# Kernel tuning notes

Hardware: AMD Instinct MI355X
Metric: run time of the kernel (lower is better)

## Reference

```python
import jax, jax.numpy as jnp
import numpy as np

EMBED_DIM = 512
POS_DIM = 192
NUM_HEADS = 8
QUERY_HEAD_DIM = 32
POS_HEAD_DIM = 4
SEQ_LEN = 1024
BATCH = 8
IN_PROJ_DIM = (QUERY_HEAD_DIM * 2 + POS_HEAD_DIM) * NUM_HEADS  # 544


def setup_inputs() -> dict:
    key = jax.random.key(0)
    ks = jax.random.split(key, 5)
    x = jax.random.normal(ks[0], (SEQ_LEN, BATCH, EMBED_DIM), dtype=jnp.float32)
    pos_emb = jax.random.normal(ks[1], (1, 2 * SEQ_LEN - 1, POS_DIM), dtype=jnp.float32)
    key_padding_mask = jnp.zeros((BATCH, SEQ_LEN), dtype=bool)
    # ScaledLinear(embed_dim, in_proj_dim) with initial_scale=query_head_dim**-0.25
    in_proj_w = jax.random.normal(ks[2], (IN_PROJ_DIM, EMBED_DIM), dtype=jnp.float32) * (EMBED_DIM ** -0.5) * (QUERY_HEAD_DIM ** -0.25)
    in_proj_b = jax.random.normal(ks[3], (IN_PROJ_DIM,), dtype=jnp.float32) * 0.01
    # ScaledLinear(pos_dim, num_heads*pos_head_dim, bias=False, initial_scale=0.05)
    linear_pos_w = jax.random.normal(ks[4], (NUM_HEADS * POS_HEAD_DIM, POS_DIM), dtype=jnp.float32) * (POS_DIM ** -0.5) * 0.05
    return {"x": x, "pos_emb": pos_emb, "key_padding_mask": key_padding_mask,
            "in_proj_w": in_proj_w, "in_proj_b": in_proj_b, "linear_pos_w": linear_pos_w}


def reference(x, pos_emb, key_padding_mask, in_proj_w, in_proj_b, linear_pos_w):
    S, B, _ = x.shape
    H, QD, PD = NUM_HEADS, QUERY_HEAD_DIM, POS_HEAD_DIM
    proj = jnp.einsum('sbe,oe->sbo', x, in_proj_w) + in_proj_b  # (S,B,544)
    qdim = H * QD
    q = proj[..., :qdim].reshape(S, B, H, QD).transpose(2, 1, 0, 3)          # (H,B,S,QD)
    k = proj[..., qdim:2 * qdim].reshape(S, B, H, QD).transpose(2, 1, 3, 0)  # (H,B,QD,S)
    p = proj[..., 2 * qdim:].reshape(S, B, H, PD).transpose(2, 1, 0, 3)      # (H,B,S,PD)
    attn_scores = jnp.matmul(q, k)  # (H,B,S,S)
    # positional scores
    pe = jnp.einsum('ltd,od->lto', pos_emb, linear_pos_w)                    # (1,2S-1,H*PD)
    pe = pe.reshape(1, 2 * S - 1, H, PD).transpose(2, 0, 3, 1)               # (H,1,PD,2S-1)
    pos_scores = jnp.matmul(p, pe)                                           # (H,B,S,2S-1)
    # rel-shift: out[h,b,i,j] = pos_scores[h,b,i, (S-1) + j - i]
    idx = (S - 1) + jnp.arange(S)[None, :] - jnp.arange(S)[:, None]          # (S,S)
    pos_scores = jnp.take_along_axis(pos_scores, idx[None, None], axis=-1)   # (H,B,S,S)
    attn_scores = attn_scores + pos_scores
    attn_scores = jnp.where(key_padding_mask[None, :, None, :], -jnp.inf, attn_scores)
    return jax.nn.softmax(attn_scores, axis=-1)
```

## Files before the change

### kernel.cpp

```cpp
#include <hip/hip_runtime.h>
#include <math.h>

#define S_LEN 1024
#define BATCH 8
#define NH 8
#define QD 32
#define PD 4
#define EMB 512
#define NPROJ 544
#define LPOS 2047

typedef __attribute__((ext_vector_type(8))) short short8;
typedef __attribute__((ext_vector_type(4))) float f32x4;
typedef __attribute__((ext_vector_type(4))) unsigned int u32x4;
typedef __attribute__((ext_vector_type(2))) unsigned int u32x2;

union U4 { u32x4 u; short8 s; };

static __device__ inline unsigned short f2bf(float f) {
    unsigned int u = __builtin_bit_cast(unsigned int, f);
    u += 0x7fffu + ((u >> 16) & 1u);
    return (unsigned short)(u >> 16);
}

#define NXV 1048576
#define NWV 69632
__global__ __launch_bounds__(256) void convert_kernel(
    const float* __restrict__ X, const float* __restrict__ W,
    unsigned short* __restrict__ Xb, unsigned short* __restrict__ Wb)
{
    int idx = blockIdx.x * 256 + threadIdx.x;
    int i = idx * 2;
    const f32x4* src;
    unsigned short* dst;
    if (i < NXV)            { src = (const f32x4*)X; dst = Xb; }
    else if (i < NXV + NWV) { src = (const f32x4*)W; dst = Wb; i -= NXV; }
    else return;
    f32x4 v0 = src[i], v1 = src[i + 1];
    union { unsigned short s[8]; u32x4 u; } pk;
    pk.s[0] = f2bf(v0.x); pk.s[1] = f2bf(v0.y);
    pk.s[2] = f2bf(v0.z); pk.s[3] = f2bf(v0.w);
    pk.s[4] = f2bf(v1.x); pk.s[5] = f2bf(v1.y);
    pk.s[6] = f2bf(v1.z); pk.s[7] = f2bf(v1.w);
    ((u32x4*)dst)[i >> 1] = pk.u;
}

#define WROW 264
__global__ __launch_bounds__(256) void proj_kernel(
    const unsigned short* __restrict__ Xb, const unsigned short* __restrict__ Wb,
    const float* __restrict__ bias,
    unsigned short* __restrict__ Qb, unsigned short* __restrict__ Kb,
    unsigned short* __restrict__ Pb)
{
    __shared__ unsigned short wlds[64 * WROW];

    const int tid = threadIdx.x;
    const int wv = tid >> 6, lane = tid & 63;
    const int n16 = lane & 15, quad = lane >> 4;
    const int m0 = blockIdx.x * 128, o0 = blockIdx.y * 64;
    const int mrow = m0 + wv * 32 + n16;
    const unsigned short* xrow = Xb + (size_t)mrow * EMB;

    f32x4 acc[2][4] = {{{0,0,0,0},{0,0,0,0},{0,0,0,0},{0,0,0,0}},
                       {{0,0,0,0},{0,0,0,0},{0,0,0,0},{0,0,0,0}}};

#pragma unroll
    for (int phase = 0; phase < 2; ++phase) {
        __syncthreads();
#pragma unroll
        for (int u = 0; u < 8; ++u) {
            int idx = tid + 256 * u;
            int r = idx >> 5, c = idx & 31;
            int o = o0 + r; if (o > NPROJ - 1) o = NPROJ - 1;
            u32x4 v = *(const u32x4*)(Wb + (size_t)o * EMB + phase * 256 + c * 8);
            *(u32x4*)(wlds + r * WROW + c * 8) = v;
        }
        __syncthreads();
#pragma unroll
        for (int kk = 0; kk < 8; ++kk) {
            const int k0 = kk * 32;
            U4 bx0; bx0.u = *(const u32x4*)(xrow + phase * 256 + k0 + quad * 8);
            U4 bx1; bx1.u = *(const u32x4*)(xrow + (size_t)16 * EMB + phase * 256 + k0 + quad * 8);
#pragma unroll
            for (int ot = 0; ot < 4; ++ot) {
                U4 aw; aw.u = *(const u32x4*)(wlds + (ot * 16 + n16) * WROW + k0 + quad * 8);
                acc[0][ot] = __builtin_amdgcn_mfma_f32_16x16x32_bf16(aw.s, bx0.s, acc[0][ot], 0, 0, 0);
                acc[1][ot] = __builtin_amdgcn_mfma_f32_16x16x32_bf16(aw.s, bx1.s, acc[1][ot], 0, 0, 0);
            }
        }
    }

#pragma unroll
    for (int g = 0; g < 2; ++g) {
        const int m = mrow + g * 16;
        const int s = m >> 3, b = m & 7;
#pragma unroll
        for (int ot = 0; ot < 4; ++ot) {
            int obase = o0 + ot * 16 + quad * 4;
            if (obase >= NPROJ) continue;
            f32x4 bv = *(const f32x4*)(bias + obase);
            union { unsigned short sh[4]; u32x2 u; } pk;
            pk.sh[0] = f2bf(acc[g][ot].x + bv.x);
            pk.sh[1] = f2bf(acc[g][ot].y + bv.y);
            pk.sh[2] = f2bf(acc[g][ot].z + bv.z);
            pk.sh[3] = f2bf(acc[g][ot].w + bv.w);
            unsigned short* dst;
            if (obase < 256) {
                int h = obase >> 5, d = obase & 31;
                dst = Qb + (((size_t)(h * BATCH + b)) * S_LEN + s) * QD + d;
            } else if (obase < 512) {
                int o2 = obase - 256;
                int h = o2 >> 5, d = o2 & 31;
                dst = Kb + (((size_t)(h * BATCH + b)) * S_LEN + s) * QD + d;
            } else {
                int h = (obase - 512) >> 2;
                dst = Pb + (((size_t)(h * BATCH + b)) * S_LEN + s) * PD;
            }
            *(u32x2*)dst = pk.u;
        }
    }
}

__global__ __launch_bounds__(256) void pe_kernel(
    const float* __restrict__ pos, const float* __restrict__ Wp,
    unsigned short* __restrict__ PEr)
{
    int o = blockIdx.x * 256 + threadIdx.x;
    if (o >= LPOS * 32) return;
    int l = o >> 5, ht = o & 31;
    const f32x4* pr = (const f32x4*)(pos + (size_t)l * 192);
    const f32x4* wr = (const f32x4*)(Wp + (size_t)ht * 192);
    float acc = 0.0f;
#pragma unroll 8
    for (int d = 0; d < 48; ++d) {
        f32x4 a = pr[d], w = wr[d];
        acc += a.x * w.x + a.y * w.y + a.z * w.z + a.w * w.w;
    }
    int h = ht >> 2, t = ht & 3, w = 2046 - l;
    PEr[((size_t)h * LPOS + w) * PD + t] = f2bf(acc);
}

__global__ __launch_bounds__(256, 3) void attn_kernel(
    const unsigned short* __restrict__ Qb, const unsigned short* __restrict__ Kb,
    const unsigned short* __restrict__ Pb, const u32x2* __restrict__ PEr,
    const unsigned char* __restrict__ mask, float* __restrict__ out)
{
    __shared__ u32x4 pe_pair[1040];
    __shared__ float madd[S_LEN];
    __shared__ float redm[4][16];
    __shared__ float reds[4][16];
    __shared__ float tbuf[4 * 1024];

    const int hb = blockIdx.y;
    const int h = hb >> 3, b = hb & 7;
    const int i0 = blockIdx.x * 16;
    const int tid = threadIdx.x;
    const int wv = tid >> 6, lane = tid & 63;
    const int n16 = lane & 15, quad = lane >> 4;

    const u32x2* src = PEr + (size_t)h * LPOS + i0;
    for (int wl = tid; wl < 1039; wl += 256) {
        u32x2 lo = src[wl];
        u32x2 hi = src[wl + 1];
        u32x4 v; v.x = lo.x; v.y = lo.y; v.z = hi.x; v.w = hi.y;
        pe_pair[wl] = v;
    }
    for (int j = tid; j < S_LEN; j += 256)
        madd[j] = mask[b * S_LEN + j] ? -INFINITY : 0.0f;

    U4 b1; b1.u = *(const u32x4*)(Qb + ((size_t)hb * S_LEN + i0 + n16) * QD + quad * 8);
    u32x2 p4 = *(const u32x2*)(Pb + ((size_t)hb * S_LEN + i0 + n16) * PD);
    U4 b2, b3;
    b2.u.x = (n16 == 2 * quad)     ? p4.x : 0u;
    b2.u.y = (n16 == 2 * quad)     ? p4.y : 0u;
    b2.u.z = (n16 == 2 * quad + 1) ? p4.x : 0u;
    b2.u.w = (n16 == 2 * quad + 1) ? p4.y : 0u;
    b3.u.x = (n16 == 2 * quad + 8) ? p4.x : 0u;
    b3.u.y = (n16 == 2 * quad + 8) ? p4.y : 0u;
    b3.u.z = (n16 == 2 * quad + 9) ? p4.x : 0u;
    b3.u.w = (n16 == 2 * quad + 9) ? p4.y : 0u;

    __syncthreads();

    f32x4 sc[16];
    const unsigned short* kbase =
        Kb + (size_t)hb * S_LEN * QD + (size_t)(wv * 256 + n16) * QD + quad * 8;
    const int wbase = 1023 - wv * 256 - n16 + 2 * quad;

#pragma unroll
    for (int t = 0; t < 16; ++t) {
        U4 a1; a1.u = *(const u32x4*)(kbase + t * 16 * QD);
        U4 a2; a2.u = pe_pair[wbase - t * 16];
        U4 a3; a3.u = pe_pair[wbase - t * 16 + 8];
        f32x4 acc = {0.0f, 0.0f, 0.0f, 0.0f};
        acc = __builtin_amdgcn_mfma_f32_16x16x32_bf16(a3.s, b3.s, acc, 0, 0, 0);
        acc = __builtin_amdgcn_mfma_f32_16x16x32_bf16(a2.s, b2.s, acc, 0, 0, 0);
        acc = __builtin_amdgcn_mfma_f32_16x16x32_bf16(a1.s, b1.s, acc, 0, 0, 0);
        sc[t] = acc + *(const f32x4*)&madd[wv * 256 + t * 16 + quad * 4];
    }

    float mx = -INFINITY;
#pragma unroll
    for (int t = 0; t < 16; ++t)
        mx = fmaxf(mx, fmaxf(fmaxf(sc[t].x, sc[t].y), fmaxf(sc[t].z, sc[t].w)));
    mx = fmaxf(mx, __shfl_xor(mx, 16));
    mx = fmaxf(mx, __shfl_xor(mx, 32));
    if (quad == 0) redm[wv][n16] = mx;
    __syncthreads();
    mx = fmaxf(fmaxf(redm[0][n16], redm[1][n16]),
               fmaxf(redm[2][n16], redm[3][n16]));

    float sum = 0.0f;
#pragma unroll
    for (int t = 0; t < 16; ++t) {
        sc[t].x = __expf(sc[t].x - mx);
        sc[t].y = __expf(sc[t].y - mx);
        sc[t].z = __expf(sc[t].z - mx);
        sc[t].w = __expf(sc[t].w - mx);
        sum += sc[t].x + sc[t].y + sc[t].z + sc[t].w;
    }
    sum += __shfl_xor(sum, 16);
    sum += __shfl_xor(sum, 32);
    if (quad == 0) reds[wv][n16] = sum;
    __syncthreads();
    const float tot = reds[0][n16] + reds[1][n16] + reds[2][n16] + reds[3][n16];
    const float inv = 1.0f / tot;

    float* wbuf = tbuf + wv * 1024;
    const int i_out_base = (int)((size_t)hb * S_LEN + i0);
#pragma unroll
    for (int c = 0; c < 4; ++c) {
#pragma unroll
        for (int tl = 0; tl < 4; ++tl) {
            f32x4 o4 = sc[c * 4 + tl] * inv;
            int phys = ((tl * 16 + quad * 4) + 4 * n16) & 63;
            *(f32x4*)&wbuf[n16 * 64 + phys] = o4;
        }
#pragma unroll
        for (int ii = 0; ii < 4; ++ii) {
            int r = (lane >> 4) + 4 * ii;
            int phys = (((lane & 15) * 4) + 4 * r) & 63;
            f32x4 v = *(const f32x4*)&wbuf[r * 64 + phys];
            float* dst = out + (size_t)(i_out_base + r) * S_LEN
                         + wv * 256 + c * 64 + (lane & 15) * 4;
            __builtin_nontemporal_store(v, (f32x4*)dst);
        }
    }
}

extern "C" void kernel_launch(void* const* d_in, const int* in_sizes, int n_in,
                              void* d_out, int out_size, void* d_ws, size_t ws_size,
                              hipStream_t stream) {
    (void)in_sizes; (void)n_in; (void)out_size; (void)ws_size;
    const float* x           = (const float*)d_in[0];
    const float* pos_emb     = (const float*)d_in[1];
    const unsigned char* msk = (const unsigned char*)d_in[2];
    const float* in_proj_w   = (const float*)d_in[3];
    const float* in_proj_b   = (const float*)d_in[4];
    const float* linear_posw = (const float*)d_in[5];
    float* out = (float*)d_out;

    char* p = (char*)d_ws;
    unsigned short* Qb  = (unsigned short*)p; p += (size_t)4 << 20;
    unsigned short* Kb  = (unsigned short*)p; p += (size_t)4 << 20;
    unsigned short* Pb  = (unsigned short*)p; p += 524288;
    unsigned short* PEr = (unsigned short*)p; p += 131072;
    unsigned short* Xb  = (unsigned short*)p; p += (size_t)8 << 20;
    unsigned short* Wb  = (unsigned short*)p; p += 557056;

    convert_kernel<<<2184, 256, 0, stream>>>(x, in_proj_w, Xb, Wb);
    pe_kernel<<<256, 256, 0, stream>>>(pos_emb, linear_posw, PEr);
    proj_kernel<<<dim3(64, 9), 256, 0, stream>>>(Xb, Wb, in_proj_b, Qb, Kb, Pb);
    attn_kernel<<<dim3(64, 64), 256, 0, stream>>>(Qb, Kb, Pb, (const u32x2*)PEr, msk, out);
}
```

Before: 324.2 us.

## Merge softmax max/sum reductions into one barrier and widen the output transpose tile

Each wave now computes its own local max and exp-sum. The per-wave max and sum are combined across waves after a single barrier by rescaling the sums, online-softmax style, which removes one block-wide __syncthreads. The PE staging buffer and the transpose buffer now alias one shared array, which is safe because pe_pair is no longer read after the barrier. The staging tile is widened so each output row write covers 128 floats instead of 64. The cost is a few extra exp evaluations per row and a larger per-wave staging region.

```diff
diff --git a/kernel.cpp b/kernel.cpp
--- a/kernel.cpp
+++ b/kernel.cpp
@@ -145,11 +145,12 @@
     const unsigned short* __restrict__ Pb, const u32x2* __restrict__ PEr,
     const unsigned char* __restrict__ mask, float* __restrict__ out)
 {
-    __shared__ u32x4 pe_pair[1040];
+    __shared__ u32x4 smem[2048];
     __shared__ float madd[S_LEN];
     __shared__ float redm[4][16];
     __shared__ float reds[4][16];
-    __shared__ float tbuf[4 * 1024];
+    u32x4* pe_pair = smem;
+    float* tbuf = (float*)smem;
 
     const int hb = blockIdx.y;
     const int h = hb >> 3, b = hb & 7;
@@ -199,50 +200,53 @@
         sc[t] = acc + *(const f32x4*)&madd[wv * 256 + t * 16 + quad * 4];
     }
 
-    float mx = -INFINITY;
+    float mxw = -INFINITY;
 #pragma unroll
     for (int t = 0; t < 16; ++t)
-        mx = fmaxf(mx, fmaxf(fmaxf(sc[t].x, sc[t].y), fmaxf(sc[t].z, sc[t].w)));
-    mx = fmaxf(mx, __shfl_xor(mx, 16));
-    mx = fmaxf(mx, __shfl_xor(mx, 32));
-    if (quad == 0) redm[wv][n16] = mx;
-    __syncthreads();
-    mx = fmaxf(fmaxf(redm[0][n16], redm[1][n16]),
-               fmaxf(redm[2][n16], redm[3][n16]));
+        mxw = fmaxf(mxw, fmaxf(fmaxf(sc[t].x, sc[t].y), fmaxf(sc[t].z, sc[t].w)));
+    mxw = fmaxf(mxw, __shfl_xor(mxw, 16));
+    mxw = fmaxf(mxw, __shfl_xor(mxw, 32));
 
     float sum = 0.0f;
 #pragma unroll
     for (int t = 0; t < 16; ++t) {
-        sc[t].x = __expf(sc[t].x - mx);
-        sc[t].y = __expf(sc[t].y - mx);
-        sc[t].z = __expf(sc[t].z - mx);
-        sc[t].w = __expf(sc[t].w - mx);
+        sc[t].x = __expf(sc[t].x - mxw);
+        sc[t].y = __expf(sc[t].y - mxw);
+        sc[t].z = __expf(sc[t].z - mxw);
+        sc[t].w = __expf(sc[t].w - mxw);
         sum += sc[t].x + sc[t].y + sc[t].z + sc[t].w;
     }
     sum += __shfl_xor(sum, 16);
     sum += __shfl_xor(sum, 32);
-    if (quad == 0) reds[wv][n16] = sum;
+    if (quad == 0) { redm[wv][n16] = mxw; reds[wv][n16] = sum; }
     __syncthreads();
-    const float tot = reds[0][n16] + reds[1][n16] + reds[2][n16] + reds[3][n16];
-    const float inv = 1.0f / tot;
-
-    float* wbuf = tbuf + wv * 1024;
+
+    const float m0_ = redm[0][n16], m1_ = redm[1][n16];
+    const float m2_ = redm[2][n16], m3_ = redm[3][n16];
+    const float m = fmaxf(fmaxf(m0_, m1_), fmaxf(m2_, m3_));
+    const float tot = reds[0][n16] * __expf(m0_ - m)
+                    + reds[1][n16] * __expf(m1_ - m)
+                    + reds[2][n16] * __expf(m2_ - m)
+                    + reds[3][n16] * __expf(m3_ - m);
+    const float scale = __expf(mxw - m) / tot;
+
+    float* wbuf = tbuf + wv * 2048;
     const int i_out_base = (int)((size_t)hb * S_LEN + i0);
 #pragma unroll
-    for (int c = 0; c < 4; ++c) {
-#pragma unroll
-        for (int tl = 0; tl < 4; ++tl) {
-            f32x4 o4 = sc[c * 4 + tl] * inv;
-            int phys = ((tl * 16 + quad * 4) + 4 * n16) & 63;
-            *(f32x4*)&wbuf[n16 * 64 + phys] = o4;
-        }
-#pragma unroll
-        for (int ii = 0; ii < 4; ++ii) {
-            int r = (lane >> 4) + 4 * ii;
-            int phys = (((lane & 15) * 4) + 4 * r) & 63;
-            f32x4 v = *(const f32x4*)&wbuf[r * 64 + phys];
+    for (int c = 0; c < 2; ++c) {
+#pragma unroll
+        for (int tl = 0; tl < 8; ++tl) {
+            f32x4 o4 = sc[c * 8 + tl] * scale;
+            int phys = ((tl * 16 + quad * 4) + 4 * n16) & 127;
+            *(f32x4*)&wbuf[n16 * 128 + phys] = o4;
+        }
+#pragma unroll
+        for (int ii = 0; ii < 8; ++ii) {
+            int r = (lane >> 5) + 2 * ii;
+            int phys = (((lane & 31) * 4) + 4 * r) & 127;
+            f32x4 v = *(const f32x4*)&wbuf[r * 128 + phys];
             float* dst = out + (size_t)(i_out_base + r) * S_LEN
-                         + wv * 256 + c * 64 + (lane & 15) * 4;
+                         + wv * 256 + c * 128 + (lane & 31) * 4;
             __builtin_nontemporal_store(v, (f32x4*)dst);
         }
     }
```

Result: no change. 322.1 us (-0.6%).
